# Performance work log

Measured on AMD Instinct MI355X. Metric: run time of the kernel, lower is better.

Reference implementation:

```python
import jax, jax.numpy as jnp
import numpy as np

ALPHA = 0.2        # APPNP teleport
LEAKY = 0.2        # leaky_relu slope in GAT
NEG_INF = -1.0e9   # additive mask value


def setup_inputs() -> dict:
    key = jax.random.key(0)
    ks = jax.random.split(key, 6)
    B, N, I, H, O = 108, 392, 256, 4, 64
    x = jax.random.normal(ks[0], (B, N, I), dtype=jnp.float32)
    # fully-connected GCN-preprocessed adjacency: D^-1/2 (A) D^-1/2 of ones == 1/N
    a = jnp.ones((N, N), dtype=jnp.float32) / N
    w_mlp = jax.random.normal(ks[1], (I, I), dtype=jnp.float32) * (1.0 / np.sqrt(I))
    b_mlp = jnp.zeros((I,), dtype=jnp.float32)
    kernel = jax.random.normal(ks[2], (I, H, O), dtype=jnp.float32) * (1.0 / np.sqrt(I))
    attn_self_k = jax.random.normal(ks[3], (O, H, 1), dtype=jnp.float32) * 0.1
    attn_neigh_k = jax.random.normal(ks[4], (O, H, 1), dtype=jnp.float32) * 0.1
    bias = jnp.zeros((H * O,), dtype=jnp.float32)
    return {"x": x, "a": a, "w_mlp": w_mlp, "b_mlp": b_mlp, "kernel": kernel,
            "attn_self_k": attn_self_k, "attn_neigh_k": attn_neigh_k, "bias": bias}


def _gnn_core(x, a, w_mlp, b_mlp, kernel, attn_self_k, attn_neigh_k, bias):
    # ---- APPNPConv (1 propagation, sigmoid MLP) ----
    mlp_out = jax.nn.sigmoid(jnp.einsum('bni,io->bno', x, w_mlp) + b_mlp)
    z = (1.0 - ALPHA) * jnp.einsum('nm,bmf->bnf', a, mlp_out) + ALPHA * mlp_out
    # ---- GATConvPatched._call_dense ----
    n = a.shape[-1]
    eye = jnp.eye(n, dtype=a.dtype)
    a_sl = jnp.where(eye > 0, jnp.ones((), a.dtype), a)   # set_diag(a, 1) = add self loops
    xp = jnp.einsum('bni,iho->bnho', z, kernel)           # [B,N,H,O]
    s = jnp.einsum('bnho,oht->bnht', xp, attn_self_k)     # [B,N,H,1]
    ng = jnp.einsum('bnho,oht->bnht', xp, attn_neigh_k)   # [B,N,H,1]
    ng_t = jnp.transpose(ng, (0, 3, 2, 1))                # '...ABC->...CBA' -> [B,1,H,N]
    coef = jax.nn.leaky_relu(s + ng_t, negative_slope=LEAKY)   # [B,N,H,N]
    mask_logits = jnp.where(a_sl == 0.0, NEG_INF, 0.0)    # [N,N]
    coef = coef + mask_logits[:, None, :]                 # broadcast over batch & heads
    attn = jax.nn.softmax(coef, axis=-1)
    # dropout is identity at inference
    out = jnp.einsum('bnhm,bmhi->bnhi', attn, xp)         # [B,N,H,O]
    B, N_, H, O = out.shape
    out = out.reshape(B, N_, H * O) + bias                # concat heads + bias
    return jax.nn.elu(out)                                # gat_activation='elu'


def reference(x, a, w_mlp, b_mlp, kernel, attn_self_k, attn_neigh_k, bias):
    return _gnn_core(x, a, w_mlp, b_mlp, kernel, attn_self_k, attn_neigh_k, bias)
```

## Files before the change

### kernel.cpp

```cpp
#include <hip/hip_runtime.h>
#include <hip/hip_bf16.h>
#include <math.h>
#include <float.h>

#define BATCH 108
#define NNODE 392
#define IDIM  256
#define HEADS 4
#define ODIM  64
#define HO    256
#define MROWS (BATCH*NNODE)
#define SGH   (BATCH*HEADS*NNODE)

typedef __attribute__((ext_vector_type(8))) short bf16x8;
typedef __attribute__((ext_vector_type(8))) unsigned short u16x8;
typedef __attribute__((ext_vector_type(4))) float f32x4;

__device__ __forceinline__ ushort f2bf(float f) {
    unsigned u = __float_as_uint(f);
    unsigned r = (u + 0x7FFFu + ((u >> 16) & 1u)) >> 16;
    return (ushort)r;
}
__device__ __forceinline__ float bf2f(ushort h) {
    return __uint_as_float(((unsigned)h) << 16);
}
__device__ __forceinline__ float fsigmoid(float x) {
    float e = __expf(-x);
    return __builtin_amdgcn_rcpf(1.0f + e);
}

#define MSTR 264

#define FRAG(src, jn, k0t) \
    (*(const bf16x8*)((src) + ((((wg * 4 + (jn)) * 8 + (k0t)) << 9)) + lane * 8))

__global__ __launch_bounds__(256)
void fused_gemm(const float* __restrict__ x, const ushort* __restrict__ wshuf,
                const ushort* __restrict__ kshuf, const float* __restrict__ bmlp,
                float* __restrict__ zbacc, ushort* __restrict__ xp0,
                const float* __restrict__ askv, const float* __restrict__ ankv,
                float* __restrict__ s0, float* __restrict__ ng0)
{
    __shared__ __attribute__((aligned(16))) ushort AsMs[32 * MSTR];
    __shared__ float cs_lds[256];

    const int t    = threadIdx.x;
    const int lane = t & 63;
    const int wg   = t >> 6;
    const int lr   = lane & 15, kq = lane >> 4;
    const int rb   = blockIdx.x;
    const int b    = blockIdx.y;
    const int row0 = rb * 32;
    const long gbase = (long)b * NNODE;

    bf16x8 wreg[2][4];
    #pragma unroll
    for (int jn = 0; jn < 4; ++jn) {
        wreg[0][jn] = FRAG(wshuf, jn, 0);
        wreg[1][jn] = FRAG(wshuf, jn, 1);
    }

    {
        const float* xb = x + (gbase + row0) * 256;
        #pragma unroll
        for (int j = 0; j < 8; ++j) {
            int e4  = t + j * 256;
            int row = e4 >> 6;
            int col = (e4 & 63) * 4;
            float4 v = (row0 + row < NNODE)
                ? *(const float4*)(xb + (long)row * 256 + col)
                : make_float4(0.f, 0.f, 0.f, 0.f);
            *(ushort4*)&AsMs[row * MSTR + col] =
                make_ushort4(f2bf(v.x), f2bf(v.y), f2bf(v.z), f2bf(v.w));
        }
    }
    __syncthreads();

    f32x4 acc[4][2] = {};

    {
        #pragma unroll
        for (int k0t = 0; k0t < 8; ++k0t) {
            bf16x8 xf0 = *(const bf16x8*)&AsMs[lr * MSTR + k0t * 32 + kq * 8];
            bf16x8 xf1 = *(const bf16x8*)&AsMs[(16 + lr) * MSTR + k0t * 32 + kq * 8];
            #pragma unroll
            for (int jn = 0; jn < 4; ++jn) {
                acc[jn][0] = __builtin_amdgcn_mfma_f32_16x16x32_bf16(
                    wreg[k0t & 1][jn], xf0, acc[jn][0], 0, 0, 0);
                acc[jn][1] = __builtin_amdgcn_mfma_f32_16x16x32_bf16(
                    wreg[k0t & 1][jn], xf1, acc[jn][1], 0, 0, 0);
            }
            if (k0t < 6) {
                #pragma unroll
                for (int jn = 0; jn < 4; ++jn)
                    wreg[k0t & 1][jn] = FRAG(wshuf, jn, k0t + 2);
            }
        }
    }

    bf16x8 kreg[2][4];
    #pragma unroll
    for (int jn = 0; jn < 4; ++jn) kreg[0][jn] = FRAG(kshuf, jn, 0);

    __syncthreads();

    {
        float4 bi[4];
        #pragma unroll
        for (int jn = 0; jn < 4; ++jn)
            bi[jn] = *(const float4*)(bmlp + 64 * wg + 16 * jn + 4 * kq);
        float cs[4][4] = {};
        #pragma unroll
        for (int imL = 0; imL < 2; ++imL) {
            const int r_ = 16 * imL + lr;
            const bool ok = row0 + r_ < NNODE;
            #pragma unroll
            for (int jn = 0; jn < 4; ++jn) {
                float v[4];
                v[0] = fsigmoid(acc[jn][imL][0] + bi[jn].x);
                v[1] = fsigmoid(acc[jn][imL][1] + bi[jn].y);
                v[2] = fsigmoid(acc[jn][imL][2] + bi[jn].z);
                v[3] = fsigmoid(acc[jn][imL][3] + bi[jn].w);
                *(ushort4*)&AsMs[r_ * MSTR + 64 * wg + 16 * jn + 4 * kq] =
                    make_ushort4(f2bf(v[0]), f2bf(v[1]), f2bf(v[2]), f2bf(v[3]));
                if (ok) {
                    cs[jn][0] += v[0]; cs[jn][1] += v[1];
                    cs[jn][2] += v[2]; cs[jn][3] += v[3];
                }
            }
        }
        #pragma unroll
        for (int jn = 0; jn < 4; ++jn)
            #pragma unroll
            for (int r = 0; r < 4; ++r) {
                float v = cs[jn][r];
                v += __shfl_xor(v, 1, 64);
                v += __shfl_xor(v, 2, 64);
                v += __shfl_xor(v, 4, 64);
                v += __shfl_xor(v, 8, 64);
                if (lr == 0)
                    cs_lds[64 * wg + 16 * jn + 4 * kq + r] = v;
            }
    }
    __syncthreads();

    #pragma unroll
    for (int jn = 0; jn < 4; ++jn)
        #pragma unroll
        for (int imL = 0; imL < 2; ++imL)
            acc[jn][imL] = f32x4{0.f, 0.f, 0.f, 0.f};

    #pragma unroll
    for (int jn = 0; jn < 4; ++jn) kreg[1][jn] = FRAG(kshuf, jn, 1);

    {
        #pragma unroll
        for (int k0t = 0; k0t < 8; ++k0t) {
            bf16x8 xf0 = *(const bf16x8*)&AsMs[lr * MSTR + k0t * 32 + kq * 8];
            bf16x8 xf1 = *(const bf16x8*)&AsMs[(16 + lr) * MSTR + k0t * 32 + kq * 8];
            #pragma unroll
            for (int jn = 0; jn < 4; ++jn) {
                acc[jn][0] = __builtin_amdgcn_mfma_f32_16x16x32_bf16(
                    kreg[k0t & 1][jn], xf0, acc[jn][0], 0, 0, 0);
                acc[jn][1] = __builtin_amdgcn_mfma_f32_16x16x32_bf16(
                    kreg[k0t & 1][jn], xf1, acc[jn][1], 0, 0, 0);
            }
            if (k0t < 6) {
                #pragma unroll
                for (int jn = 0; jn < 4; ++jn)
                    kreg[k0t & 1][jn] = FRAG(kshuf, jn, k0t + 2);
            }
        }
    }

    {
        const int h = wg;
        float askr[4][4], ankr[4][4];
        #pragma unroll
        for (int jn = 0; jn < 4; ++jn)
            #pragma unroll
            for (int r = 0; r < 4; ++r) {
                int o = 16 * jn + 4 * kq + r;
                askr[jn][r] = askv[o * HEADS + h];
                ankr[jn][r] = ankv[o * HEADS + h];
            }
        #pragma unroll
        for (int imL = 0; imL < 2; ++imL) {
            const int r_ = 16 * imL + lr;
            const int lrow = row0 + r_;
            const bool ok = lrow < NNODE;
            float ps = 0.0f, pn = 0.0f;
            if (ok) {
                ushort* dst = xp0 + (gbase + lrow) * 256 + 64 * h + 4 * kq;
                #pragma unroll
                for (int jn = 0; jn < 4; ++jn) {
                    float v0 = 0.2f * acc[jn][imL][0];
                    float v1 = 0.2f * acc[jn][imL][1];
                    float v2 = 0.2f * acc[jn][imL][2];
                    float v3 = 0.2f * acc[jn][imL][3];
                    *(ushort4*)(dst + 16 * jn) =
                        make_ushort4(f2bf(v0), f2bf(v1), f2bf(v2), f2bf(v3));
                    ps += v0 * askr[jn][0] + v1 * askr[jn][1] +
                          v2 * askr[jn][2] + v3 * askr[jn][3];
                    pn += v0 * ankr[jn][0] + v1 * ankr[jn][1] +
                          v2 * ankr[jn][2] + v3 * ankr[jn][3];
                }
            }
            ps += __shfl_xor(ps, 16, 64);
            ps += __shfl_xor(ps, 32, 64);
            pn += __shfl_xor(pn, 16, 64);
            pn += __shfl_xor(pn, 32, 64);
            if (ok && kq == 0) {
                long si = ((long)b * HEADS + h) * NNODE + lrow;
                s0[si]  = ps;
                ng0[si] = pn;
            }
        }
    }

    atomicAdd(&zbacc[b * 256 + t], cs_lds[t]);
}

__global__ __launch_bounds__(256)
void wcvt(const float* __restrict__ w_mlp, const float* __restrict__ kern,
          ushort* __restrict__ wshuf, ushort* __restrict__ kshuf,
          float* __restrict__ zbacc)
{
    if (blockIdx.x < BATCH)
        zbacc[blockIdx.x * 256 + threadIdx.x] = 0.0f;
    long idx = (long)(blockIdx.x & 255) * 256 + threadIdx.x;
    const float* src = (blockIdx.x < 256) ? w_mlp : kern;
    ushort* dst = (blockIdx.x < 256) ? wshuf : kshuf;
    int e    = idx & 7;
    int lane = (int)(idx >> 3) & 63;
    int k0t  = (int)(idx >> 9) & 7;
    int jn   = (int)(idx >> 12) & 3;
    int g    = (int)(idx >> 14);
    int n = 64 * g + 16 * jn + (lane & 15);
    int k = 32 * k0t + (lane >> 4) * 8 + e;
    dst[idx] = f2bf(src[(long)k * 256 + n]);
}

#define NP  (NNODE + 1)
__global__ __launch_bounds__(512)
void attn_fused(const float* __restrict__ s0, const float* __restrict__ ng0,
                const float* __restrict__ zbacc, const float* __restrict__ kern,
                const float* __restrict__ askv, const float* __restrict__ ankv,
                const ushort* __restrict__ xp, const float* __restrict__ bias,
                float* __restrict__ out)
{
    __shared__ float  key[512];
    __shared__ int    perm[512];
    __shared__ float  w1[NNODE], w2[NNODE];
    __shared__ float  D1[NNODE + 1], D2[NNODE + 1];
    __shared__ float  g1s[NNODE], g2s[NNODE];
    __shared__ ushort tls[NNODE];
    __shared__ float  biasl[64];
    __shared__ float  Vs[8 * NP];
    __shared__ float  S1[8 * NP];
    __shared__ float  CT[64][9], CT2[64][9];
    __shared__ float  zsh[IDIM];
    __shared__ float  partK[8][64];
    __shared__ float  wsumA[8], wsumB[8];
    __shared__ float  scs[2];

    const int t  = threadIdx.x;
    const int bh = blockIdx.x;
    const int b  = bh >> 2, h = bh & 3;
    const long base = (long)bh * NNODE;
    const int ln = t & 63, w = t >> 6;

    if (t < IDIM) zsh[t] = zbacc[b * 256 + t] * (0.8f / (float)NNODE);
    __syncthreads();
    {
        float p = 0.0f;
        #pragma unroll
        for (int kk = 0; kk < 32; ++kk) {
            int k = w * 32 + kk;
            p = fmaf(zsh[k], kern[(long)k * HO + h * 64 + ln], p);
        }
        partK[w][ln] = p;
    }
    __syncthreads();
    if (t < 64) {
        float zk = 0.0f;
        #pragma unroll
        for (int kc = 0; kc < 8; ++kc) zk += partK[kc][t];
        biasl[t] = bias[h * 64 + t] + zk;
        float ps = zk * askv[t * HEADS + h];
        float pn = zk * ankv[t * HEADS + h];
        #pragma unroll
        for (int off = 32; off; off >>= 1) {
            ps += __shfl_down(ps, off, 64);
            pn += __shfl_down(pn, off, 64);
        }
        if (t == 0) { scs[0] = ps; scs[1] = pn; }
    }
    __syncthreads();
    const float sc = scs[0], ngc = scs[1];

    float rk = (t < NNODE) ? (ng0[base + t] + ngc) : FLT_MAX;
    int   rp = t;

    for (int k = 2; k <= 512; k <<= 1) {
        for (int j = k >> 1; j > 0; j >>= 1) {
            const bool dir = ((t & k) == 0);
            const bool lower = ((t & j) == 0);
            float ok_; int op;
            if (j >= 64) {
                __syncthreads();
                key[t] = rk; perm[t] = rp;
                __syncthreads();
                ok_ = key[t ^ j];
                op  = perm[t ^ j];
            } else {
                ok_ = __shfl_xor(rk, j, 64);
                op  = __shfl_xor(rp, j, 64);
            }
            const bool sw = lower ? ((rk > ok_) == dir) : ((ok_ > rk) == dir);
            if (sw) { rk = ok_; rp = op; }
        }
    }
    __syncthreads();
    key[t] = rk; perm[t] = rp;

    const float w1v = (t < NNODE) ? __expf(rk) : 0.0f;
    const float w2v = (t < NNODE) ? __expf(0.2f * rk) : 0.0f;
    if (t < NNODE) { w1[t] = w1v; w2[t] = w2v; }

    float v1 = w1v;
    #pragma unroll
    for (int s = 1; s < 64; s <<= 1) {
        float tmp = __shfl_down(v1, s, 64);
        if (ln + s < 64) v1 += tmp;
    }
    float v2 = (ln >= 1) ? __shfl_up(w2v, 1, 64) : 0.0f;
    #pragma unroll
    for (int s = 1; s < 64; s <<= 1) {
        float tmp = __shfl_up(v2, s, 64);
        if (ln >= s) v2 += tmp;
    }
    const float wt2 = __shfl(v2, 63, 64) + __shfl(w2v, 63, 64);
    if (ln == 0) { wsumA[w] = v1; wsumB[w] = wt2; }
    __syncthreads();
    {
        float off1 = 0.0f, off2 = 0.0f;
        for (int ww = w + 1; ww < 8; ++ww) off1 += wsumA[ww];
        for (int ww = 0; ww < w; ++ww)     off2 += wsumB[ww];
        if (t < NNODE) {
            D1[t] = v1 + off1;
            D2[t] = v2 + off2;
        }
        if (t == 0) {
            D1[NNODE] = 0.0f;
            float tot = 0.0f;
            #pragma unroll
            for (int ww = 0; ww < 8; ++ww) tot += wsumB[ww];
            D2[NNODE] = tot;
        }
    }
    __syncthreads();

    if (t < NNODE) {
        float sn = s0[base + t] + sc;
        float negs = -sn;
        int lo = 0, hi = NNODE;
        while (lo < hi) {
            int mid = (lo + hi) >> 1;
            if (key[mid] < negs) lo = mid + 1; else hi = mid;
        }
        float e1 = __expf(sn), e2 = __expf(0.2f * sn);
        float inv = __builtin_amdgcn_rcpf(e1 * D1[lo] + e2 * D2[lo]);
        g1s[t] = e1 * inv;
        g2s[t] = e2 * inv;
        tls[t] = (ushort)lo;
    }
    __syncthreads();

    const int c = t >> 3, o = t & 7;
    for (int og2 = 0; og2 < 8; ++og2) {
        const int c0 = h * 64 + og2 * 8;

        if (t < NNODE) {
            int m = perm[t];
            u16x8 raw = *(const u16x8*)(xp + ((long)b * NNODE + m) * HO + c0);
            #pragma unroll
            for (int oo = 0; oo < 8; ++oo) Vs[oo * NP + t] = bf2f(raw[oo]);
        }
        __syncthreads();

        {
            float acc = 0.0f;
            #pragma unroll
            for (int jj = 7 - 1; jj >= 0; --jj) {
                int j = c * 7 + jj;
                if (j < NNODE) {
                    acc = fmaf(w1[j], Vs[o * NP + j], acc);
                    S1[o * NP + j] = acc;
                }
            }
            CT[c][o] = acc;
        }
        __syncthreads();
        {
            float v = CT[ln][w];
            #pragma unroll
            for (int s = 1; s < 64; s <<= 1) {
                float tmp = __shfl_down(v, s, 64);
                if (ln + s < 64) v += tmp;
            }
            CT[ln][w] = v;
        }
        __syncthreads();
        {
            float off = (c < 63) ? CT[c + 1][o] : 0.0f;
            #pragma unroll
            for (int jj = 0; jj < 7; ++jj) {
                int j = c * 7 + jj;
                if (j < NNODE) S1[o * NP + j] += off;
            }
            if (c == 0) S1[o * NP + NNODE] = 0.0f;
        }
        {
            float acc = 0.0f;
            #pragma unroll
            for (int jj = 0; jj < 7; ++jj) {
                int j = c * 7 + jj;
                if (j < NNODE) {
                    float tmp = Vs[o * NP + j];
                    Vs[o * NP + j] = acc;
                    acc = fmaf(w2[j], tmp, acc);
                }
            }
            CT2[c][o] = acc;
        }
        __syncthreads();
        {
            float v = CT2[ln][w];
            #pragma unroll
            for (int s = 1; s < 64; s <<= 1) {
                float tmp = __shfl_up(v, s, 64);
                if (ln >= s) v += tmp;
            }
            CT2[ln][w] = v;
        }
        __syncthreads();
        {
            float off = (c > 0) ? CT2[c - 1][o] : 0.0f;
            #pragma unroll
            for (int jj = 0; jj < 7; ++jj) {
                int j = c * 7 + jj;
                if (j < NNODE) Vs[o * NP + j] += off;
            }
            if (c == 63) Vs[o * NP + NNODE] = CT2[63][o];
        }
        __syncthreads();

        for (int idx = t; idx < NNODE * 2; idx += 512) {
            int n = idx >> 1, q = (idx & 1) * 4;
            int tt = tls[n];
            float g1 = g1s[n], g2 = g2s[n];
            float r[4];
            #pragma unroll
            for (int rr = 0; rr < 4; ++rr) {
                int oo = q + rr;
                float v = g1 * S1[oo * NP + tt] + g2 * Vs[oo * NP + tt] +
                          biasl[og2 * 8 + oo];
                r[rr] = (v > 0.0f) ? v : (__expf(v) - 1.0f);
            }
            *(float4*)(out + ((long)b * NNODE + n) * HO + c0 + q) =
                make_float4(r[0], r[1], r[2], r[3]);
        }
        __syncthreads();
    }
}

extern "C" void kernel_launch(void* const* d_in, const int* in_sizes, int n_in,
                              void* d_out, int out_size, void* d_ws, size_t ws_size,
                              hipStream_t stream) {
    const float* x     = (const float*)d_in[0];
    const float* w_mlp = (const float*)d_in[2];
    const float* b_mlp = (const float*)d_in[3];
    const float* kern  = (const float*)d_in[4];
    const float* ask   = (const float*)d_in[5];
    const float* ank   = (const float*)d_in[6];
    const float* bias  = (const float*)d_in[7];
    float* out = (float*)d_out;

    const long TENS = (long)MROWS * IDIM;
    float*  s0    = (float*)d_ws;
    float*  ng0   = s0 + SGH;
    float*  zbacc = ng0 + SGH;
    ushort* xp_bf = (ushort*)(zbacc + (long)BATCH * IDIM);
    ushort* wshuf = xp_bf + TENS;
    ushort* kshuf = wshuf + 65536;

    dim3 blk(256);

    wcvt<<<dim3(512), blk, 0, stream>>>(w_mlp, kern, wshuf, kshuf, zbacc);

    fused_gemm<<<dim3(13, BATCH), dim3(256), 0, stream>>>(
        x, wshuf, kshuf, b_mlp, zbacc, xp_bf, ask, ank, s0, ng0);

    attn_fused<<<dim3(BATCH * HEADS), dim3(512), 0, stream>>>(
        s0, ng0, zbacc, kern, ask, ank, xp_bf, bias, out);
}
```

Measured before the change: 183.5 us.

## Widen attention block to 1024 threads, 16-column chunks, prefetch next chunk

The fused attention kernel now runs 1024 threads per (batch, head) block and processes 16 output columns per iteration instead of 8. That halves the loop trip count and the number of barriers per chunk. The gather of the next xp chunk from global memory is issued into registers before the current chunk's scan, overlapping load latency with compute. In exchange it doubles the LDS buffers, leaves half the threads idle during the sort and scan phases, and may lower occupancy and raise register pressure.

New measurement: 173.0 us. 5.7% less time.

```diff
diff --git a/kernel.cpp b/kernel.cpp
--- a/kernel.cpp
+++ b/kernel.cpp
@@ -242,7 +242,7 @@
 }
 
 #define NP  (NNODE + 1)
-__global__ __launch_bounds__(512)
+__global__ __launch_bounds__(1024)
 void attn_fused(const float* __restrict__ s0, const float* __restrict__ ng0,
                 const float* __restrict__ zbacc, const float* __restrict__ kern,
                 const float* __restrict__ askv, const float* __restrict__ ankv,
@@ -256,11 +256,11 @@
     __shared__ float  g1s[NNODE], g2s[NNODE];
     __shared__ ushort tls[NNODE];
     __shared__ float  biasl[64];
-    __shared__ float  Vs[8 * NP];
-    __shared__ float  S1[8 * NP];
-    __shared__ float  CT[64][9], CT2[64][9];
+    __shared__ float  Vs[16 * NP];
+    __shared__ float  S1[16 * NP];
+    __shared__ float  CT[64][17], CT2[64][17];
     __shared__ float  zsh[IDIM];
-    __shared__ float  partK[8][64];
+    __shared__ float  partK[16][64];
     __shared__ float  wsumA[8], wsumB[8];
     __shared__ float  scs[2];
 
@@ -275,8 +275,8 @@
     {
         float p = 0.0f;
         #pragma unroll
-        for (int kk = 0; kk < 32; ++kk) {
-            int k = w * 32 + kk;
+        for (int kk = 0; kk < 16; ++kk) {
+            int k = w * 16 + kk;
             p = fmaf(zsh[k], kern[(long)k * HO + h * 64 + ln], p);
         }
         partK[w][ln] = p;
@@ -285,7 +285,7 @@
     if (t < 64) {
         float zk = 0.0f;
         #pragma unroll
-        for (int kc = 0; kc < 8; ++kc) zk += partK[kc][t];
+        for (int kc = 0; kc < 16; ++kc) zk += partK[kc][t];
         biasl[t] = bias[h * 64 + t] + zk;
         float ps = zk * askv[t * HEADS + h];
         float pn = zk * ankv[t * HEADS + h];
@@ -304,46 +304,67 @@
 
     for (int k = 2; k <= 512; k <<= 1) {
         for (int j = k >> 1; j > 0; j >>= 1) {
-            const bool dir = ((t & k) == 0);
-            const bool lower = ((t & j) == 0);
-            float ok_; int op;
             if (j >= 64) {
                 __syncthreads();
-                key[t] = rk; perm[t] = rp;
+                if (t < 512) { key[t] = rk; perm[t] = rp; }
                 __syncthreads();
-                ok_ = key[t ^ j];
-                op  = perm[t ^ j];
+                if (t < 512) {
+                    const bool dir = ((t & k) == 0);
+                    const bool lower = ((t & j) == 0);
+                    float ok_ = key[t ^ j];
+                    int   op  = perm[t ^ j];
+                    const bool sw = lower ? ((rk > ok_) == dir)
+                                          : ((ok_ > rk) == dir);
+                    if (sw) { rk = ok_; rp = op; }
+                }
             } else {
-                ok_ = __shfl_xor(rk, j, 64);
-                op  = __shfl_xor(rp, j, 64);
-            }
-            const bool sw = lower ? ((rk > ok_) == dir) : ((ok_ > rk) == dir);
-            if (sw) { rk = ok_; rp = op; }
-        }
-    }
-    __syncthreads();
-    key[t] = rk; perm[t] = rp;
+                if (t < 512) {
+                    const bool dir = ((t & k) == 0);
+                    const bool lower = ((t & j) == 0);
+                    float ok_ = __shfl_xor(rk, j, 64);
+                    int   op  = __shfl_xor(rp, j, 64);
+                    const bool sw = lower ? ((rk > ok_) == dir)
+                                          : ((ok_ > rk) == dir);
+                    if (sw) { rk = ok_; rp = op; }
+                }
+            }
+        }
+    }
+    __syncthreads();
+    if (t < 512) { key[t] = rk; perm[t] = rp; }
 
     const float w1v = (t < NNODE) ? __expf(rk) : 0.0f;
     const float w2v = (t < NNODE) ? __expf(0.2f * rk) : 0.0f;
     if (t < NNODE) { w1[t] = w1v; w2[t] = w2v; }
 
-    float v1 = w1v;
-    #pragma unroll
-    for (int s = 1; s < 64; s <<= 1) {
-        float tmp = __shfl_down(v1, s, 64);
-        if (ln + s < 64) v1 += tmp;
-    }
-    float v2 = (ln >= 1) ? __shfl_up(w2v, 1, 64) : 0.0f;
-    #pragma unroll
-    for (int s = 1; s < 64; s <<= 1) {
-        float tmp = __shfl_up(v2, s, 64);
-        if (ln >= s) v2 += tmp;
-    }
-    const float wt2 = __shfl(v2, 63, 64) + __shfl(w2v, 63, 64);
-    if (ln == 0) { wsumA[w] = v1; wsumB[w] = wt2; }
-    __syncthreads();
-    {
+    float v1 = w1v, v2 = 0.0f;
+    if (t < 512) {
+        #pragma unroll
+        for (int s = 1; s < 64; s <<= 1) {
+            float tmp = __shfl_down(v1, s, 64);
+            if (ln + s < 64) v1 += tmp;
+        }
+        v2 = (ln >= 1) ? __shfl_up(w2v, 1, 64) : 0.0f;
+        #pragma unroll
+        for (int s = 1; s < 64; s <<= 1) {
+            float tmp = __shfl_up(v2, s, 64);
+            if (ln >= s) v2 += tmp;
+        }
+        const float wt2 = __shfl(v2, 63, 64) + __shfl(w2v, 63, 64);
+        if (ln == 0) { wsumA[w] = v1; wsumB[w] = wt2; }
+    }
+    __syncthreads();
+
+    u16x8 raw;
+    const bool gt = (t < NNODE * 2);
+    const int gj = t >> 1, gq = (t & 1) * 8;
+    int grow = 0;
+    if (gt) {
+        grow = perm[gj];
+        raw = *(const u16x8*)(xp + ((long)b * NNODE + grow) * HO + h * 64 + gq);
+    }
+
+    if (t < 512) {
         float off1 = 0.0f, off2 = 0.0f;
         for (int ww = w + 1; ww < 8; ++ww) off1 += wsumA[ww];
         for (int ww = 0; ww < w; ++ww)     off2 += wsumB[ww];
@@ -377,22 +398,23 @@
     }
     __syncthreads();
 
-    const int c = t >> 3, o = t & 7;
-    for (int og2 = 0; og2 < 8; ++og2) {
-        const int c0 = h * 64 + og2 * 8;
-
-        if (t < NNODE) {
-            int m = perm[t];
-            u16x8 raw = *(const u16x8*)(xp + ((long)b * NNODE + m) * HO + c0);
-            #pragma unroll
-            for (int oo = 0; oo < 8; ++oo) Vs[oo * NP + t] = bf2f(raw[oo]);
-        }
-        __syncthreads();
+    const int c = t >> 4, o = t & 15;
+    for (int og2 = 0; og2 < 4; ++og2) {
+        const int c0 = h * 64 + og2 * 16;
+
+        if (gt) {
+            #pragma unroll
+            for (int oo = 0; oo < 8; ++oo) Vs[(gq + oo) * NP + gj] = bf2f(raw[oo]);
+        }
+        __syncthreads();
+        if (og2 < 3 && gt)
+            raw = *(const u16x8*)(xp + ((long)b * NNODE + grow) * HO +
+                                  h * 64 + (og2 + 1) * 16 + gq);
 
         {
             float acc = 0.0f;
             #pragma unroll
-            for (int jj = 7 - 1; jj >= 0; --jj) {
+            for (int jj = 6; jj >= 0; --jj) {
                 int j = c * 7 + jj;
                 if (j < NNODE) {
                     acc = fmaf(w1[j], Vs[o * NP + j], acc);
@@ -456,8 +478,8 @@
         }
         __syncthreads();
 
-        for (int idx = t; idx < NNODE * 2; idx += 512) {
-            int n = idx >> 1, q = (idx & 1) * 4;
+        for (int idx = t; idx < NNODE * 4; idx += 1024) {
+            int n = idx >> 2, q = (idx & 3) * 4;
             int tt = tls[n];
             float g1 = g1s[n], g2 = g2s[n];
             float r[4];
@@ -465,7 +487,7 @@
             for (int rr = 0; rr < 4; ++rr) {
                 int oo = q + rr;
                 float v = g1 * S1[oo * NP + tt] + g2 * Vs[oo * NP + tt] +
-                          biasl[og2 * 8 + oo];
+                          biasl[og2 * 16 + oo];
                 r[rr] = (v > 0.0f) ? v : (__expf(v) - 1.0f);
             }
             *(float4*)(out + ((long)b * NNODE + n) * HO + c0 + q) =
@@ -502,6 +524,6 @@
     fused_gemm<<<dim3(13, BATCH), dim3(256), 0, stream>>>(
         x, wshuf, kshuf, b_mlp, zbacc, xp_bf, ask, ank, s0, ng0);
 
-    attn_fused<<<dim3(BATCH * HEADS), dim3(512), 0, stream>>>(
+    attn_fused<<<dim3(BATCH * HEADS), dim3(1024), 0, stream>>>(
         s0, ng0, zbacc, kern, ask, ank, xp_bf, bias, out);
 }
```
